# Kernel tuning notes

Measured on AMD Instinct MI355X. Metric: run time of the kernel, lower is better.

## Reference

```python
import jax, jax.numpy as jnp
import numpy as np

B, N, D = 4, 4096, 128


def setup_inputs() -> dict:
    key = jax.random.key(0)
    k1, k2, k3 = jax.random.split(key, 3)
    x = jax.random.normal(k1, (B, N, D), dtype=jnp.float32)
    # random 0/1 adjacency (float, matching torch usage where adj>0 is masked)
    adj_mat = jax.random.randint(k2, (B, N, N), 0, 2).astype(jnp.float32)
    # xavier_normal_ for square [D, D]: std = sqrt(2 / (D + D))
    U = jax.random.normal(k3, (D, D), dtype=jnp.float32) * np.sqrt(2.0 / (D + D))
    return {"x": x, "adj_mat": adj_mat, "U": U}


def reference(x, adj_mat, U):
    # per-node loop in the original is equivalent to a masked adj^T matmul:
    # new_x[b,i,:] = relu( (sum_j 1[adj[b,j,i] > 0] * x[b,j,:]) @ U / deg[b,i] )
    # with deg = adj.sum(axis=1), i.e. deg[b,i] = sum_j adj[b,j,i].
    mask = (adj_mat > 0).astype(x.dtype)            # [B, N, N]
    deg = jnp.sum(adj_mat, axis=1)                  # [B, N]
    agg = jnp.einsum("bji,bjd->bid", mask, x)       # [B, N, D]
    out = jax.nn.relu(jnp.einsum("bid,de->bie", agg, U) / deg[..., None])
    return out
```

## Files before the change

### kernel.cpp

```cpp
#include <hip/hip_runtime.h>
#include <hip/hip_bf16.h>
#include <stdint.h>

#define BB 4
#define NN 4096
#define DD 128
#define BI 64
#define BJ 64
#define NT (NN / BJ)

typedef _Float16 f16;
typedef __attribute__((ext_vector_type(8))) _Float16 f16x8;
typedef __attribute__((ext_vector_type(4))) float f32x4;

typedef __attribute__((address_space(3))) uint32_t lds_u32_t;
typedef const __attribute__((address_space(1))) uint32_t glb_u32_t;

__device__ __forceinline__ void gload_lds16(const void* g, void* l) {
    __builtin_amdgcn_global_load_lds((glb_u32_t*)g, (lds_u32_t*)l, 16, 0, 0);
}

__global__ void prep_xt(const float* __restrict__ x, f16* __restrict__ xt) {
    __shared__ float tile[32][33];
    int bid = blockIdx.x;
    int b = bid >> 9;
    int rest = bid & 511;
    int j0 = (rest >> 2) * 32;
    int d0 = (rest & 3) * 32;
    int t = threadIdx.x;
#pragma unroll
    for (int p = 0; p < 4; ++p) {
        int idx = p * 256 + t;
        int jj = idx >> 5, dd = idx & 31;
        tile[jj][dd] = x[((size_t)b * NN + j0 + jj) * DD + d0 + dd];
    }
    __syncthreads();
#pragma unroll
    for (int p = 0; p < 4; ++p) {
        int idx = p * 256 + t;
        int dd = idx >> 5, jj = idx & 31;
        xt[((size_t)b * DD + d0 + dd) * NN + j0 + jj] = (f16)tile[jj][dd];
    }
}

__global__ void prep_ut(const float* __restrict__ U, f16* __restrict__ ut) {
    __shared__ float tile[32][33];
    int bid = blockIdx.x;
    int d0 = (bid >> 2) * 32, e0 = (bid & 3) * 32;
    int t = threadIdx.x;
#pragma unroll
    for (int p = 0; p < 4; ++p) {
        int idx = p * 256 + t;
        int dd = idx >> 5, ee = idx & 31;
        tile[dd][ee] = U[(size_t)(d0 + dd) * DD + e0 + ee];
    }
    __syncthreads();
#pragma unroll
    for (int p = 0; p < 4; ++p) {
        int idx = p * 256 + t;
        int ee = idx >> 5, dd = idx & 31;
        ut[(size_t)(e0 + ee) * DD + d0 + dd] = (f16)tile[dd][ee];
    }
}

__global__ __launch_bounds__(512, 2) void fused_kernel(
    const float* __restrict__ adj, const f16* __restrict__ xt,
    const f16* __restrict__ ut, float* __restrict__ out)
{
    __shared__ __align__(16) f16 mlds[2][BI * BJ];
    __shared__ __align__(16) f16 xlds[2][DD * BJ];
    __shared__ float degl[8][BI];
    __shared__ float degs[BI];

    const int t = threadIdx.x;
    const int w = t >> 6;
    const int l = t & 63;
    const int bid = blockIdx.x;
    const int b = bid >> 6;
    const int i0 = (bid & 63) * BI;

    const float* adjb = adj + (size_t)b * NN * NN + i0;
    const f16* xtb = xt + (size_t)b * DD * NN;

    const int si = l;
    const int su = w;
    const int mwoff = (si * 8 + (su ^ ((si >> 1) & 7))) * 8;

    const int ifr = (w & 3) * 16;
    const int dbase = (w >> 2) * 64;

    f32x4 acc[4] = {f32x4{0,0,0,0}, f32x4{0,0,0,0}, f32x4{0,0,0,0}, f32x4{0,0,0,0}};
    float degp = 0.f;
    float v[8];

    auto load_adj = [&](int jt) {
        const float* src = adjb + (size_t)(jt * BJ + su * 8) * NN + si;
#pragma unroll
        for (int q = 0; q < 8; ++q) v[q] = src[(size_t)q * NN];
    };
    auto dma_xt = [&](int jt, int buf) {
        const int j0 = jt * BJ;
#pragma unroll
        for (int c = 0; c < 2; ++c) {
            int g = (w * 2 + c) * 64 + l;
            int d = g >> 3, ul = g & 7;
            int ug = ul ^ ((d >> 1) & 7);
            gload_lds16(xtb + (size_t)d * NN + j0 + ug * 8, &xlds[buf][(size_t)g * 8]);
        }
    };
    auto convert_write = [&](int buf) {
        f16x8 m8;
#pragma unroll
        for (int q = 0; q < 8; ++q) {
            degp += v[q];
            m8[q] = v[q] > 0.f ? (f16)1.f : (f16)0.f;
        }
        *(f16x8*)&mlds[buf][mwoff] = m8;
    };
    auto compute = [&](int buf) {
#pragma unroll
        for (int kk = 0; kk < 2; ++kk) {
            const int row = ifr + (l & 15);
            const int ug = kk * 4 + (l >> 4);
            f16x8 a = *(const f16x8*)&mlds[buf][(row * 8 + (ug ^ ((row >> 1) & 7))) * 8];
#pragma unroll
            for (int f = 0; f < 4; ++f) {
                const int d = dbase + f * 16 + (l & 15);
                f16x8 bb = *(const f16x8*)&xlds[buf][(d * 8 + (ug ^ ((d >> 1) & 7))) * 8];
                acc[f] = __builtin_amdgcn_mfma_f32_16x16x32_f16(a, bb, acc[f], 0, 0, 0);
            }
        }
    };

    load_adj(0);
    dma_xt(0, 0);
    convert_write(0);
    __syncthreads();

    for (int jt = 0; jt < NT; ++jt) {
        const int cur = jt & 1;
        if (jt + 1 < NT) {
            load_adj(jt + 1);
            dma_xt(jt + 1, cur ^ 1);
        }
        compute(cur);
        if (jt + 1 < NT) convert_write(cur ^ 1);
        __syncthreads();
    }

    degl[w][l] = degp;
    __syncthreads();

    f16* alds = &mlds[0][0];
    f16* ulds = &xlds[0][0];

#pragma unroll
    for (int c = 0; c < 4; ++c) {
        int g = (w * 4 + c) * 64 + l;
        int e = g >> 4, ul = g & 15;
        int ug = ul ^ (e & 7);
        gload_lds16(ut + (size_t)e * DD + ug * 8, &ulds[(size_t)g * 8]);
    }
#pragma unroll
    for (int f = 0; f < 4; ++f) {
#pragma unroll
        for (int r = 0; r < 4; ++r) {
            int row = ifr + (l >> 4) * 4 + r;
            int col = dbase + f * 16 + (l & 15);
            alds[(row * 16 + ((col >> 3) ^ (row & 7))) * 8 + (col & 7)] = (f16)acc[f][r];
        }
    }
    if (t < BI) {
        float s = 0.f;
#pragma unroll
        for (int q = 0; q < 8; ++q) s += degl[q][t];
        degs[t] = s;
    }
    __syncthreads();

    const int ifr2 = (w & 3) * 16;
    const int ebase = (w >> 2) * 64;
    f32x4 acc2[4] = {f32x4{0,0,0,0}, f32x4{0,0,0,0}, f32x4{0,0,0,0}, f32x4{0,0,0,0}};
#pragma unroll
    for (int kk = 0; kk < 4; ++kk) {
        const int row = ifr2 + (l & 15);
        const int ug = kk * 4 + (l >> 4);
        f16x8 a = *(const f16x8*)&alds[(row * 16 + (ug ^ (row & 7))) * 8];
#pragma unroll
        for (int ef = 0; ef < 4; ++ef) {
            const int e = ebase + ef * 16 + (l & 15);
            f16x8 bb = *(const f16x8*)&ulds[(e * 16 + (ug ^ (e & 7))) * 8];
            acc2[ef] = __builtin_amdgcn_mfma_f32_16x16x32_f16(a, bb, acc2[ef], 0, 0, 0);
        }
    }

    float rdeg[4];
#pragma unroll
    for (int r = 0; r < 4; ++r)
        rdeg[r] = 1.0f / degs[ifr2 + (l >> 4) * 4 + r];

    float* outb = out + ((size_t)b * NN + i0) * DD;
#pragma unroll
    for (int ef = 0; ef < 4; ++ef) {
#pragma unroll
        for (int r = 0; r < 4; ++r) {
            int row = ifr2 + (l >> 4) * 4 + r;
            int e = ebase + ef * 16 + (l & 15);
            float vv = acc2[ef][r] * rdeg[r];
            outb[(size_t)row * DD + e] = vv > 0.f ? vv : 0.f;
        }
    }
}

extern "C" void kernel_launch(void* const* d_in, const int* in_sizes, int n_in,
                              void* d_out, int out_size, void* d_ws, size_t ws_size,
                              hipStream_t stream) {
    const float* x   = (const float*)d_in[0];
    const float* adj = (const float*)d_in[1];
    const float* U   = (const float*)d_in[2];
    float* out = (float*)d_out;

    char* ws = (char*)d_ws;
    f16* xt = (f16*)ws;
    f16* ut = (f16*)(ws + (size_t)BB * DD * NN * 2);

    hipLaunchKernelGGL(prep_xt, dim3(BB * (NN / 32) * (DD / 32)), dim3(256), 0, stream, x, xt);
    hipLaunchKernelGGL(prep_ut, dim3((DD / 32) * (DD / 32)), dim3(256), 0, stream, U, ut);
    hipLaunchKernelGGL(fused_kernel, dim3(BB * (NN / BI)), dim3(512), 0, stream, adj, xt, ut, out);
}
```

Measured before the change: 383.0 us.

## Halve row tile to 32 and double block count for better occupancy

Reduces the i-tile per block from 64 to 32 rows, doubling the grid to 512 blocks. Warp work mapping, mask layout in LDS, and the degree reduction are reworked so each warp handles a 16x32 output fragment. Launch bounds rise to 4 blocks per CU to hide the latency of the strided adjacency loads. The cost is that x^T is reloaded twice as often, with more total LDS traffic and smaller per-warp MFMA work.

```diff
diff --git a/kernel.cpp b/kernel.cpp
--- a/kernel.cpp
+++ b/kernel.cpp
@@ -5,11 +5,12 @@
 #define BB 4
 #define NN 4096
 #define DD 128
-#define BI 64
+#define BI 32
 #define BJ 64
 #define NT (NN / BJ)
 
 typedef _Float16 f16;
+typedef __attribute__((ext_vector_type(4))) _Float16 f16x4;
 typedef __attribute__((ext_vector_type(8))) _Float16 f16x8;
 typedef __attribute__((ext_vector_type(4))) float f32x4;
 
@@ -63,40 +64,41 @@
     }
 }
 
-__global__ __launch_bounds__(512, 2) void fused_kernel(
+__global__ __launch_bounds__(512, 4) void fused_kernel(
     const float* __restrict__ adj, const f16* __restrict__ xt,
     const f16* __restrict__ ut, float* __restrict__ out)
 {
     __shared__ __align__(16) f16 mlds[2][BI * BJ];
     __shared__ __align__(16) f16 xlds[2][DD * BJ];
-    __shared__ float degl[8][BI];
+    __shared__ float degl[16][BI];
     __shared__ float degs[BI];
 
     const int t = threadIdx.x;
     const int w = t >> 6;
     const int l = t & 63;
     const int bid = blockIdx.x;
-    const int b = bid >> 6;
-    const int i0 = (bid & 63) * BI;
+    const int b = bid >> 7;
+    const int i0 = (bid & 127) * BI;
 
     const float* adjb = adj + (size_t)b * NN * NN + i0;
     const f16* xtb = xt + (size_t)b * DD * NN;
 
-    const int si = l;
-    const int su = w;
-    const int mwoff = (si * 8 + (su ^ ((si >> 1) & 7))) * 8;
-
-    const int ifr = (w & 3) * 16;
-    const int dbase = (w >> 2) * 64;
-
-    f32x4 acc[4] = {f32x4{0,0,0,0}, f32x4{0,0,0,0}, f32x4{0,0,0,0}, f32x4{0,0,0,0}};
+    const int si = l & 31;
+    const int jg = w * 2 + (l >> 5);
+    const int physu = (jg >> 1) ^ ((si >> 1) & 7);
+    const int mwoff = (si * 8 + physu) * 8 + (jg & 1) * 4;
+
+    const int iw = w & 1;
+    const int dq = w >> 1;
+
+    f32x4 acc[2] = {f32x4{0,0,0,0}, f32x4{0,0,0,0}};
     float degp = 0.f;
-    float v[8];
+    float v[4];
 
     auto load_adj = [&](int jt) {
-        const float* src = adjb + (size_t)(jt * BJ + su * 8) * NN + si;
-#pragma unroll
-        for (int q = 0; q < 8; ++q) v[q] = src[(size_t)q * NN];
+        const float* src = adjb + (size_t)(jt * BJ + jg * 4) * NN + si;
+#pragma unroll
+        for (int q = 0; q < 4; ++q) v[q] = src[(size_t)q * NN];
     };
     auto dma_xt = [&](int jt, int buf) {
         const int j0 = jt * BJ;
@@ -109,23 +111,23 @@
         }
     };
     auto convert_write = [&](int buf) {
-        f16x8 m8;
-#pragma unroll
-        for (int q = 0; q < 8; ++q) {
+        f16x4 m4;
+#pragma unroll
+        for (int q = 0; q < 4; ++q) {
             degp += v[q];
-            m8[q] = v[q] > 0.f ? (f16)1.f : (f16)0.f;
-        }
-        *(f16x8*)&mlds[buf][mwoff] = m8;
+            m4[q] = v[q] > 0.f ? (f16)1.f : (f16)0.f;
+        }
+        *(f16x4*)&mlds[buf][mwoff] = m4;
     };
     auto compute = [&](int buf) {
 #pragma unroll
         for (int kk = 0; kk < 2; ++kk) {
-            const int row = ifr + (l & 15);
+            const int row = iw * 16 + (l & 15);
             const int ug = kk * 4 + (l >> 4);
             f16x8 a = *(const f16x8*)&mlds[buf][(row * 8 + (ug ^ ((row >> 1) & 7))) * 8];
 #pragma unroll
-            for (int f = 0; f < 4; ++f) {
-                const int d = dbase + f * 16 + (l & 15);
+            for (int f = 0; f < 2; ++f) {
+                const int d = dq * 32 + f * 16 + (l & 15);
                 f16x8 bb = *(const f16x8*)&xlds[buf][(d * 8 + (ug ^ ((d >> 1) & 7))) * 8];
                 acc[f] = __builtin_amdgcn_mfma_f32_16x16x32_f16(a, bb, acc[f], 0, 0, 0);
             }
@@ -148,7 +150,7 @@
         __syncthreads();
     }
 
-    degl[w][l] = degp;
+    degl[jg][si] = degp;
     __syncthreads();
 
     f16* alds = &mlds[0][0];
@@ -162,32 +164,32 @@
         gload_lds16(ut + (size_t)e * DD + ug * 8, &ulds[(size_t)g * 8]);
     }
 #pragma unroll
-    for (int f = 0; f < 4; ++f) {
+    for (int f = 0; f < 2; ++f) {
 #pragma unroll
         for (int r = 0; r < 4; ++r) {
-            int row = ifr + (l >> 4) * 4 + r;
-            int col = dbase + f * 16 + (l & 15);
+            int row = iw * 16 + (l >> 4) * 4 + r;
+            int col = dq * 32 + f * 16 + (l & 15);
             alds[(row * 16 + ((col >> 3) ^ (row & 7))) * 8 + (col & 7)] = (f16)acc[f][r];
         }
     }
     if (t < BI) {
         float s = 0.f;
 #pragma unroll
-        for (int q = 0; q < 8; ++q) s += degl[q][t];
+        for (int q = 0; q < 16; ++q) s += degl[q][t];
         degs[t] = s;
     }
     __syncthreads();
 
-    const int ifr2 = (w & 3) * 16;
-    const int ebase = (w >> 2) * 64;
-    f32x4 acc2[4] = {f32x4{0,0,0,0}, f32x4{0,0,0,0}, f32x4{0,0,0,0}, f32x4{0,0,0,0}};
+    const int iw2 = w & 1;
+    const int ebase = (w >> 1) * 32;
+    f32x4 acc2[2] = {f32x4{0,0,0,0}, f32x4{0,0,0,0}};
 #pragma unroll
     for (int kk = 0; kk < 4; ++kk) {
-        const int row = ifr2 + (l & 15);
+        const int row = iw2 * 16 + (l & 15);
         const int ug = kk * 4 + (l >> 4);
         f16x8 a = *(const f16x8*)&alds[(row * 16 + (ug ^ (row & 7))) * 8];
 #pragma unroll
-        for (int ef = 0; ef < 4; ++ef) {
+        for (int ef = 0; ef < 2; ++ef) {
             const int e = ebase + ef * 16 + (l & 15);
             f16x8 bb = *(const f16x8*)&ulds[(e * 16 + (ug ^ (e & 7))) * 8];
             acc2[ef] = __builtin_amdgcn_mfma_f32_16x16x32_f16(a, bb, acc2[ef], 0, 0, 0);
@@ -197,14 +199,14 @@
     float rdeg[4];
 #pragma unroll
     for (int r = 0; r < 4; ++r)
-        rdeg[r] = 1.0f / degs[ifr2 + (l >> 4) * 4 + r];
+        rdeg[r] = 1.0f / degs[iw2 * 16 + (l >> 4) * 4 + r];
 
     float* outb = out + ((size_t)b * NN + i0) * DD;
 #pragma unroll
-    for (int ef = 0; ef < 4; ++ef) {
+    for (int ef = 0; ef < 2; ++ef) {
 #pragma unroll
         for (int r = 0; r < 4; ++r) {
-            int row = ifr2 + (l >> 4) * 4 + r;
+            int row = iw2 * 16 + (l >> 4) * 4 + r;
             int e = ebase + ef * 16 + (l & 15);
             float vv = acc2[ef][r] * rdeg[r];
             outb[(size_t)row * DD + e] = vv > 0.f ? vv : 0.f;
```

Result: no change. 383.3 us (+0.1%).
